# Optimization experiments

Measured on AMD Instinct MI355X. Metric: run time of the kernel, lower is better.

## Reference

```python
import jax, jax.numpy as jnp
import numpy as np

H, W = 5, 11          # fixed spatial map from ConvLSTM2D((5,11), ...)
P = H * W             # 55 pixels; 1x1 convs are per-pixel linear layers
HC = 64               # hidden channels
IC = 2                # input channels
FC_DIMS = [2 * HC * P, 3400, 1000, 500, 50]  # 7040 -> 3400 -> 1000 -> 500 -> 50


def setup_inputs() -> dict:
    key = jax.random.key(0)
    ks = jax.random.split(key, 24)
    B, T = 32, 256
    s = 0.05
    d = {}
    d["x1"] = jax.random.normal(ks[0], (B, T, IC, H, W), jnp.float32)
    d["x2"] = jax.random.normal(ks[1], (B, T, IC, H, W), jnp.float32)
    # ConvLSTM cell params: 1x1 convs fused into (in, 4*HC) matrices, gate order i,f,o,g
    d["wx1"] = jax.random.normal(ks[2], (IC, 4 * HC), jnp.float32) * s
    d["wh1"] = jax.random.normal(ks[3], (HC, 4 * HC), jnp.float32) * s
    d["bx1"] = jax.random.normal(ks[4], (4 * HC,), jnp.float32) * s
    d["bh1"] = jax.random.normal(ks[5], (4 * HC,), jnp.float32) * s
    d["wx2"] = jax.random.normal(ks[6], (IC, 4 * HC), jnp.float32) * s
    d["wh2"] = jax.random.normal(ks[7], (HC, 4 * HC), jnp.float32) * s
    d["bx2"] = jax.random.normal(ks[8], (4 * HC,), jnp.float32) * s
    d["bh2"] = jax.random.normal(ks[9], (4 * HC,), jnp.float32) * s
    # FC stack (stored as (in,out) so y = x @ W + b, equivalent to torch Linear)
    for i in range(4):
        fan_in, fan_out = FC_DIMS[i], FC_DIMS[i + 1]
        lim = 1.0 / np.sqrt(fan_in)
        d[f"fw{i+2}"] = jax.random.uniform(ks[10 + 2 * i], (fan_in, fan_out), jnp.float32, -lim, lim)
        d[f"fb{i+2}"] = jax.random.uniform(ks[11 + 2 * i], (fan_out,), jnp.float32, -lim, lim)
    return d


def _cell_step(h, c, gx, wh, bh):
    # gx: (B,P,4*HC) precomputed x contribution; h,c: (B,P,HC)
    g = gx + h @ wh + bh
    i, f, o, gg = jnp.split(g, 4, axis=-1)
    c = jax.nn.sigmoid(f) * c + jax.nn.sigmoid(i) * jnp.tanh(gg)
    h = jax.nn.sigmoid(o) * jnp.tanh(c)
    return h, c


def _sub_forward(x, wx1, wh1, bx1, bh1, wx2, wh2, bx2, bh2,
                 fw2, fb2, fw3, fb3, fw4, fb4, fw5, fb5):
    B, T = x.shape[0], x.shape[1]
    # (B,T,C,H,W) -> (B,T,P,C): pixels become a batch dim for the 1x1 convs
    xs = x.transpose(0, 1, 3, 4, 2).reshape(B, T, P, IC)
    # Precompute all input-to-gate projections once (big batched GEMM)
    gx1 = jnp.einsum('btpc,cd->btpd', xs, wx1) + bx1            # cell1: forward in time
    gx2 = jnp.einsum('btpc,cd->btpd', xs[:, ::-1], wx2) + bx2   # cell2: reversed in time
    h0 = jnp.zeros((B, P, HC), x.dtype)

    def step(carry, g):
        h1, c1, h2, c2 = carry
        g1, g2 = g
        h1, c1 = _cell_step(h1, c1, g1, wh1, bh1)
        h2, c2 = _cell_step(h2, c2, g2, wh2, bh2)
        return (h1, c1, h2, c2), None

    (h1, _, h2, _), _ = jax.lax.scan(
        step, (h0, h0, h0, h0),
        (gx1.transpose(1, 0, 2, 3), gx2.transpose(1, 0, 2, 3)))

    # torch.cat((h1,h2),1) on (B,HC,H,W) then flatten -> channel-major layout
    out = jnp.concatenate([h1.transpose(0, 2, 1), h2.transpose(0, 2, 1)], axis=1).reshape(B, -1)
    out = out @ fw2 + fb2
    out = out @ fw3 + fb3
    out = out @ fw4 + fb4
    out = out @ fw5 + fb5
    return out


def reference(x1, x2, wx1, wh1, bx1, bh1, wx2, wh2, bx2, bh2,
              fw2, fb2, fw3, fb3, fw4, fb4, fw5, fb5):
    args = (wx1, wh1, bx1, bh1, wx2, wh2, bx2, bh2,
            fw2, fb2, fw3, fb3, fw4, fb4, fw5, fb5)
    out1 = _sub_forward(x1, *args)
    out2 = _sub_forward(x2, *args)
    return (out1, out2)
```

## Files before the change

### kernel.cpp

```cpp
#include <hip/hip_runtime.h>


#define T_STEPS 256
#define PIX 55
#define MT 16
#define TILES 110
#define LOG2E 1.4426950408889634f
#define FC_SUB 128
#define FC_GRP 16

typedef float f32x4 __attribute__((ext_vector_type(4)));
typedef __bf16 bf16x8 __attribute__((ext_vector_type(8)));
typedef __bf16 bf16x4 __attribute__((ext_vector_type(4)));

__global__ __launch_bounds__(256) void lstm_kernel(
    const float* __restrict__ x1, const float* __restrict__ x2,
    const float* __restrict__ wx1, const float* __restrict__ wh1,
    const float* __restrict__ bx1, const float* __restrict__ bh1,
    const float* __restrict__ wx2, const float* __restrict__ wh2,
    const float* __restrict__ bx2, const float* __restrict__ bh2,
    float* __restrict__ feat)
{
    int bid  = blockIdx.x;
    int tile = bid % TILES;
    int cc   = bid / TILES;
    int sub  = cc >> 1, cell = cc & 1;
    const float* x  = sub  ? x2  : x1;
    const float* wx = cell ? wx2 : wx1;
    const float* wh = cell ? wh2 : wh1;
    const float* bx = cell ? bx2 : bx1;
    const float* bh = cell ? bh2 : bh1;

    int tid  = threadIdx.x;
    int w    = tid >> 6;
    int l    = tid & 63;
    int quad = l >> 4;
    int c16  = l & 15;

    __shared__ float xl[MT * 514];
    __shared__ __align__(16) __bf16 hb[2][2][MT][72];

    {
        int seq0 = tile * MT;
        for (int i = 0; i < 32; ++i) {
            int idx = tid + 256 * i;
            int m = idx >> 9;
            int tc = idx & 511;
            int t = tc >> 1, c = tc & 1;
            int seq = seq0 + m;
            int b = seq / PIX, p = seq % PIX;
            xl[m * 514 + tc] = x[((b * T_STEPS + t) * 2 + c) * PIX + p];
        }
    }
    {
        __bf16* hz = &hb[0][0][0][0];
        for (int i = tid; i < 2 * 2 * MT * 72; i += 256) hz[i] = (__bf16)0.0f;
    }

    bf16x8 Whi[4][2], Wlo[4][2];
    float btot[4][4], wxa[4][4], wxb[4][4];
#pragma unroll
    for (int g = 0; g < 4; ++g) {
        int col = 64 * g + 16 * w + c16;
#pragma unroll
        for (int r = 0; r < 4; ++r) {
            int u = 64 * g + 16 * w + 4 * quad + r;
            btot[g][r] = bx[u] + bh[u];
            wxa[g][r]  = wx[u];
            wxb[g][r]  = wx[256 + u];
        }
#pragma unroll
        for (int q = 0; q < 2; ++q) {
#pragma unroll
            for (int j = 0; j < 8; ++j) {
                int k = 32 * q + 8 * quad + j;
                float wv = wh[k * 256 + col];
                __bf16 hi = (__bf16)wv;
                Whi[g][q][j] = hi;
                Wlo[g][q][j] = (__bf16)(wv - (float)hi);
            }
        }
    }

    float cst[4]  = {0.f, 0.f, 0.f, 0.f};
    float hfin[4] = {0.f, 0.f, 0.f, 0.f};

    __syncthreads();

    for (int t = 0; t < T_STEPS; ++t) {
        int rb = t & 1, wb = rb ^ 1;
        int tx = cell ? (T_STEPS - 1 - t) : t;

        bf16x8 Bh[2], Bl[2];
#pragma unroll
        for (int q = 0; q < 2; ++q) {
            Bh[q] = *(const bf16x8*)&hb[rb][0][c16][32 * q + 8 * quad];
            Bl[q] = *(const bf16x8*)&hb[rb][1][c16][32 * q + 8 * quad];
        }
        float2 xv = *(const float2*)&xl[c16 * 514 + tx * 2];

        f32x4 acc[4];
#pragma unroll
        for (int g = 0; g < 4; ++g) {
#pragma unroll
            for (int r = 0; r < 4; ++r)
                acc[g][r] = fmaf(xv.y, wxb[g][r], fmaf(xv.x, wxa[g][r], btot[g][r]));
        }
#pragma unroll
        for (int g = 0; g < 4; ++g) {
            acc[g] = __builtin_amdgcn_mfma_f32_16x16x32_bf16(Whi[g][0], Bh[0], acc[g], 0, 0, 0);
            acc[g] = __builtin_amdgcn_mfma_f32_16x16x32_bf16(Whi[g][1], Bh[1], acc[g], 0, 0, 0);
            acc[g] = __builtin_amdgcn_mfma_f32_16x16x32_bf16(Wlo[g][0], Bh[0], acc[g], 0, 0, 0);
            acc[g] = __builtin_amdgcn_mfma_f32_16x16x32_bf16(Wlo[g][1], Bh[1], acc[g], 0, 0, 0);
            acc[g] = __builtin_amdgcn_mfma_f32_16x16x32_bf16(Whi[g][0], Bl[0], acc[g], 0, 0, 0);
            acc[g] = __builtin_amdgcn_mfma_f32_16x16x32_bf16(Whi[g][1], Bl[1], acc[g], 0, 0, 0);
        }

        bf16x4 ph, pl;
#pragma unroll
        for (int r = 0; r < 4; ++r) {
            float iv = acc[0][r], fv = acc[1][r], ov = acc[2][r], gv = acc[3][r];
            float ei = __builtin_amdgcn_exp2f(-LOG2E * iv);
            float ef = __builtin_amdgcn_exp2f(-LOG2E * fv);
            float eo = __builtin_amdgcn_exp2f(-LOG2E * ov);
            float eg = __builtin_amdgcn_exp2f(-2.0f * LOG2E * gv);
            float sf  = __builtin_amdgcn_rcpf(1.0f + ef);
            float itg = (1.0f - eg) * __builtin_amdgcn_rcpf((1.0f + ei) * (1.0f + eg));
            float c   = fmaf(sf, cst[r], itg);
            cst[r] = c;
            float ec = __builtin_amdgcn_exp2f(-2.0f * LOG2E * c);
            float h  = (1.0f - ec) * __builtin_amdgcn_rcpf((1.0f + eo) * (1.0f + ec));
            hfin[r] = h;
            __bf16 hi = (__bf16)h;
            ph[r] = hi;
            pl[r] = (__bf16)(h - (float)hi);
        }
        *(bf16x4*)&hb[wb][0][c16][16 * w + 4 * quad] = ph;
        *(bf16x4*)&hb[wb][1][c16][16 * w + 4 * quad] = pl;
        __syncthreads();
    }

    {
        int seq = tile * MT + c16;
        int b = seq / PIX, p = seq % PIX;
#pragma unroll
        for (int r = 0; r < 4; ++r) {
            int u = 16 * w + 4 * quad + r;
            feat[(size_t)(sub * 32 + b) * 7040 + (cell * 64 + u) * PIX + p] = hfin[r];
        }
    }
}

__global__ __launch_bounds__(256) void fc_gemm(const float* __restrict__ A,
                                               const float* __restrict__ W,
                                               float* __restrict__ part,
                                               int K, int N, int kchunk) {
    __shared__ __align__(16) float al[FC_SUB * 68];
    int tid = threadIdx.x;
    int l   = tid & 63;
    int wv  = tid >> 6;
    int k0   = blockIdx.y * kchunk;
    int kend = min(K, k0 + kchunk);

    int n  = blockIdx.x * 64 + l;
    int ne = min(n, N - 1);

    float acc[16];
#pragma unroll
    for (int i = 0; i < 16; ++i) acc[i] = 0.0f;

    for (int ks = k0; ks < kend; ks += FC_SUB) {
        int kcur = min(FC_SUB, kend - ks);
        __syncthreads();
        if (kcur == FC_SUB) {
#pragma unroll
            for (int i = 0; i < 32; ++i) {
                int idx = tid + 256 * i;
                int m = idx >> 7, kc = idx & 127;
                al[kc * 68 + m] = A[(size_t)m * K + ks + kc];
            }
        } else {
#pragma unroll
            for (int i = 0; i < 32; ++i) {
                int idx = tid + 256 * i;
                int m = idx >> 7, kc = idx & 127;
                if (kc < kcur) al[kc * 68 + m] = A[(size_t)m * K + ks + kc];
            }
        }
        __syncthreads();

        const float* wr = W + (size_t)ks * N + ne;
        int kc0 = 0;
        for (; kc0 + FC_GRP <= kcur; kc0 += FC_GRP) {
            float wbuf[FC_GRP];
#pragma unroll
            for (int j = 0; j < FC_GRP; ++j)
                wbuf[j] = wr[(size_t)(kc0 + j) * N];
#pragma unroll
            for (int j = 0; j < FC_GRP; ++j) {
                const float4* ap = (const float4*)&al[(kc0 + j) * 68 + 16 * wv];
#pragma unroll
                for (int i = 0; i < 4; ++i) {
                    float4 a = ap[i];
                    acc[4 * i + 0] = fmaf(a.x, wbuf[j], acc[4 * i + 0]);
                    acc[4 * i + 1] = fmaf(a.y, wbuf[j], acc[4 * i + 1]);
                    acc[4 * i + 2] = fmaf(a.z, wbuf[j], acc[4 * i + 2]);
                    acc[4 * i + 3] = fmaf(a.w, wbuf[j], acc[4 * i + 3]);
                }
            }
        }
        for (; kc0 < kcur; ++kc0) {
            float wvv = wr[(size_t)kc0 * N];
            const float4* ap = (const float4*)&al[kc0 * 68 + 16 * wv];
#pragma unroll
            for (int i = 0; i < 4; ++i) {
                float4 a = ap[i];
                acc[4 * i + 0] = fmaf(a.x, wvv, acc[4 * i + 0]);
                acc[4 * i + 1] = fmaf(a.y, wvv, acc[4 * i + 1]);
                acc[4 * i + 2] = fmaf(a.z, wvv, acc[4 * i + 2]);
                acc[4 * i + 3] = fmaf(a.w, wvv, acc[4 * i + 3]);
            }
        }
    }

    if (n < N) {
        float* pr = part + (size_t)blockIdx.y * 64 * N + n;
#pragma unroll
        for (int i = 0; i < 16; ++i)
            pr[(size_t)(16 * wv + i) * N] = acc[i];
    }
}

__global__ __launch_bounds__(256) void fc_reduce(const float* __restrict__ part,
                                                 const float* __restrict__ bias,
                                                 float* __restrict__ out,
                                                 int S, int N) {
    int n = blockIdx.x * 256 + threadIdx.x;
    int m = blockIdx.y;
    if (n >= N) return;
    float s = bias[n];
    for (int i = 0; i < S; ++i)
        s += part[(size_t)i * 64 * N + (size_t)m * N + n];
    out[(size_t)m * N + n] = s;
}

extern "C" void kernel_launch(void* const* d_in, const int* in_sizes, int n_in,
                              void* d_out, int out_size, void* d_ws, size_t ws_size,
                              hipStream_t stream) {
    const float* x1  = (const float*)d_in[0];
    const float* x2  = (const float*)d_in[1];
    const float* wx1 = (const float*)d_in[2];
    const float* wh1 = (const float*)d_in[3];
    const float* bx1 = (const float*)d_in[4];
    const float* bh1 = (const float*)d_in[5];
    const float* wx2 = (const float*)d_in[6];
    const float* wh2 = (const float*)d_in[7];
    const float* bx2 = (const float*)d_in[8];
    const float* bh2 = (const float*)d_in[9];
    const float* fw2 = (const float*)d_in[10];
    const float* fb2 = (const float*)d_in[11];
    const float* fw3 = (const float*)d_in[12];
    const float* fb3 = (const float*)d_in[13];
    const float* fw4 = (const float*)d_in[14];
    const float* fb4 = (const float*)d_in[15];
    const float* fw5 = (const float*)d_in[16];
    const float* fb5 = (const float*)d_in[17];

    char* ws = (char*)d_ws;
    float* feat = (float*)ws;
    float* t1   = feat + (size_t)64 * 7040;
    float* t2   = t1   + (size_t)64 * 3400;
    float* t3   = t2   + (size_t)64 * 1000;
    float* part = t3   + (size_t)64 * 500;
    float* o    = (float*)d_out;

    lstm_kernel<<<dim3(440), dim3(256), 0, stream>>>(
        x1, x2, wx1, wh1, bx1, bh1, wx2, wh2, bx2, bh2, feat);

    fc_gemm<<<dim3(54, 14), dim3(256), 0, stream>>>(feat, fw2, part, 7040, 3400, 512);
    fc_reduce<<<dim3(14, 64), dim3(256), 0, stream>>>(part, fb2, t1, 14, 3400);

    fc_gemm<<<dim3(16, 27), dim3(256), 0, stream>>>(t1, fw3, part, 3400, 1000, 128);
    fc_reduce<<<dim3(4, 64), dim3(256), 0, stream>>>(part, fb3, t2, 27, 1000);

    fc_gemm<<<dim3(8, 8), dim3(256), 0, stream>>>(t2, fw4, part, 1000, 500, 128);
    fc_reduce<<<dim3(2, 64), dim3(256), 0, stream>>>(part, fb4, t3, 8, 500);

    fc_gemm<<<dim3(1, 4), dim3(256), 0, stream>>>(t3, fw5, part, 500, 50, 128);
    fc_reduce<<<dim3(1, 64), dim3(256), 0, stream>>>(part, fb5, o, 4, 50);
}
```

Baseline: 590.6 us.

## Prefetch LSTM inputs, interleave MFMA chains, and widen FC GEMM to two columns

The LSTM step loop now loads the next timestep's input before the barrier and is unrolled by two. The MFMA calls are reordered so the four gate accumulators form independent chains instead of six dependent calls per gate, and the exponentials are computed in a separate batch before the gate math. The FC GEMM has each lane compute two output columns with float2 weight loads and stores, which halves the grid width and reuses each shared-memory A value twice. This raises register pressure and assumes N is even for aligned float2 access.

```diff
diff --git a/kernel.cpp b/kernel.cpp
--- a/kernel.cpp
+++ b/kernel.cpp
@@ -86,10 +86,11 @@
     float hfin[4] = {0.f, 0.f, 0.f, 0.f};
 
     __syncthreads();
-
+    float2 xv = *(const float2*)&xl[c16 * 514 + (cell ? (T_STEPS - 1) : 0) * 2];
+
+#pragma unroll 2
     for (int t = 0; t < T_STEPS; ++t) {
         int rb = t & 1, wb = rb ^ 1;
-        int tx = cell ? (T_STEPS - 1 - t) : t;
 
         bf16x8 Bh[2], Bl[2];
 #pragma unroll
@@ -97,7 +98,6 @@
             Bh[q] = *(const bf16x8*)&hb[rb][0][c16][32 * q + 8 * quad];
             Bl[q] = *(const bf16x8*)&hb[rb][1][c16][32 * q + 8 * quad];
         }
-        float2 xv = *(const float2*)&xl[c16 * 514 + tx * 2];
 
         f32x4 acc[4];
 #pragma unroll
@@ -107,29 +107,42 @@
                 acc[g][r] = fmaf(xv.y, wxb[g][r], fmaf(xv.x, wxa[g][r], btot[g][r]));
         }
 #pragma unroll
-        for (int g = 0; g < 4; ++g) {
+        for (int g = 0; g < 4; ++g)
             acc[g] = __builtin_amdgcn_mfma_f32_16x16x32_bf16(Whi[g][0], Bh[0], acc[g], 0, 0, 0);
+#pragma unroll
+        for (int g = 0; g < 4; ++g)
             acc[g] = __builtin_amdgcn_mfma_f32_16x16x32_bf16(Whi[g][1], Bh[1], acc[g], 0, 0, 0);
+#pragma unroll
+        for (int g = 0; g < 4; ++g)
             acc[g] = __builtin_amdgcn_mfma_f32_16x16x32_bf16(Wlo[g][0], Bh[0], acc[g], 0, 0, 0);
+#pragma unroll
+        for (int g = 0; g < 4; ++g)
             acc[g] = __builtin_amdgcn_mfma_f32_16x16x32_bf16(Wlo[g][1], Bh[1], acc[g], 0, 0, 0);
+#pragma unroll
+        for (int g = 0; g < 4; ++g)
             acc[g] = __builtin_amdgcn_mfma_f32_16x16x32_bf16(Whi[g][0], Bl[0], acc[g], 0, 0, 0);
+#pragma unroll
+        for (int g = 0; g < 4; ++g)
             acc[g] = __builtin_amdgcn_mfma_f32_16x16x32_bf16(Whi[g][1], Bl[1], acc[g], 0, 0, 0);
+
+        float ei[4], ef[4], eo[4], eg[4];
+#pragma unroll
+        for (int r = 0; r < 4; ++r) {
+            ei[r] = __builtin_amdgcn_exp2f(-LOG2E * acc[0][r]);
+            ef[r] = __builtin_amdgcn_exp2f(-LOG2E * acc[1][r]);
+            eo[r] = __builtin_amdgcn_exp2f(-LOG2E * acc[2][r]);
+            eg[r] = __builtin_amdgcn_exp2f(-2.0f * LOG2E * acc[3][r]);
         }
 
         bf16x4 ph, pl;
 #pragma unroll
         for (int r = 0; r < 4; ++r) {
-            float iv = acc[0][r], fv = acc[1][r], ov = acc[2][r], gv = acc[3][r];
-            float ei = __builtin_amdgcn_exp2f(-LOG2E * iv);
-            float ef = __builtin_amdgcn_exp2f(-LOG2E * fv);
-            float eo = __builtin_amdgcn_exp2f(-LOG2E * ov);
-            float eg = __builtin_amdgcn_exp2f(-2.0f * LOG2E * gv);
-            float sf  = __builtin_amdgcn_rcpf(1.0f + ef);
-            float itg = (1.0f - eg) * __builtin_amdgcn_rcpf((1.0f + ei) * (1.0f + eg));
+            float sf  = __builtin_amdgcn_rcpf(1.0f + ef[r]);
+            float itg = (1.0f - eg[r]) * __builtin_amdgcn_rcpf((1.0f + ei[r]) * (1.0f + eg[r]));
             float c   = fmaf(sf, cst[r], itg);
             cst[r] = c;
             float ec = __builtin_amdgcn_exp2f(-2.0f * LOG2E * c);
-            float h  = (1.0f - ec) * __builtin_amdgcn_rcpf((1.0f + eo) * (1.0f + ec));
+            float h  = (1.0f - ec) * __builtin_amdgcn_rcpf((1.0f + eo[r]) * (1.0f + ec));
             hfin[r] = h;
             __bf16 hi = (__bf16)h;
             ph[r] = hi;
@@ -137,6 +150,11 @@
         }
         *(bf16x4*)&hb[wb][0][c16][16 * w + 4 * quad] = ph;
         *(bf16x4*)&hb[wb][1][c16][16 * w + 4 * quad] = pl;
+
+        {
+            int txn = (cell ? (T_STEPS - 2 - t) : (t + 1)) & 255;
+            xv = *(const float2*)&xl[c16 * 514 + txn * 2];
+        }
         __syncthreads();
     }
 
@@ -162,12 +180,12 @@
     int k0   = blockIdx.y * kchunk;
     int kend = min(K, k0 + kchunk);
 
-    int n  = blockIdx.x * 64 + l;
-    int ne = min(n, N - 1);
-
-    float acc[16];
-#pragma unroll
-    for (int i = 0; i < 16; ++i) acc[i] = 0.0f;
+    int n  = blockIdx.x * 128 + 2 * l;
+    int ne = min(n, N - 2);
+
+    float2 acc[16];
+#pragma unroll
+    for (int i = 0; i < 16; ++i) acc[i] = make_float2(0.0f, 0.0f);
 
     for (int ks = k0; ks < kend; ks += FC_SUB) {
         int kcur = min(FC_SUB, kend - ks);
@@ -192,33 +210,41 @@
         const float* wr = W + (size_t)ks * N + ne;
         int kc0 = 0;
         for (; kc0 + FC_GRP <= kcur; kc0 += FC_GRP) {
-            float wbuf[FC_GRP];
+            float2 wbuf[FC_GRP];
 #pragma unroll
             for (int j = 0; j < FC_GRP; ++j)
-                wbuf[j] = wr[(size_t)(kc0 + j) * N];
+                wbuf[j] = *(const float2*)&wr[(size_t)(kc0 + j) * N];
 #pragma unroll
             for (int j = 0; j < FC_GRP; ++j) {
                 const float4* ap = (const float4*)&al[(kc0 + j) * 68 + 16 * wv];
 #pragma unroll
                 for (int i = 0; i < 4; ++i) {
                     float4 a = ap[i];
-                    acc[4 * i + 0] = fmaf(a.x, wbuf[j], acc[4 * i + 0]);
-                    acc[4 * i + 1] = fmaf(a.y, wbuf[j], acc[4 * i + 1]);
-                    acc[4 * i + 2] = fmaf(a.z, wbuf[j], acc[4 * i + 2]);
-                    acc[4 * i + 3] = fmaf(a.w, wbuf[j], acc[4 * i + 3]);
+                    acc[4 * i + 0].x = fmaf(a.x, wbuf[j].x, acc[4 * i + 0].x);
+                    acc[4 * i + 0].y = fmaf(a.x, wbuf[j].y, acc[4 * i + 0].y);
+                    acc[4 * i + 1].x = fmaf(a.y, wbuf[j].x, acc[4 * i + 1].x);
+                    acc[4 * i + 1].y = fmaf(a.y, wbuf[j].y, acc[4 * i + 1].y);
+                    acc[4 * i + 2].x = fmaf(a.z, wbuf[j].x, acc[4 * i + 2].x);
+                    acc[4 * i + 2].y = fmaf(a.z, wbuf[j].y, acc[4 * i + 2].y);
+                    acc[4 * i + 3].x = fmaf(a.w, wbuf[j].x, acc[4 * i + 3].x);
+                    acc[4 * i + 3].y = fmaf(a.w, wbuf[j].y, acc[4 * i + 3].y);
                 }
             }
         }
         for (; kc0 < kcur; ++kc0) {
-            float wvv = wr[(size_t)kc0 * N];
+            float2 wvv = *(const float2*)&wr[(size_t)kc0 * N];
             const float4* ap = (const float4*)&al[kc0 * 68 + 16 * wv];
 #pragma unroll
             for (int i = 0; i < 4; ++i) {
                 float4 a = ap[i];
-                acc[4 * i + 0] = fmaf(a.x, wvv, acc[4 * i + 0]);
-                acc[4 * i + 1] = fmaf(a.y, wvv, acc[4 * i + 1]);
-                acc[4 * i + 2] = fmaf(a.z, wvv, acc[4 * i + 2]);
-                acc[4 * i + 3] = fmaf(a.w, wvv, acc[4 * i + 3]);
+                acc[4 * i + 0].x = fmaf(a.x, wvv.x, acc[4 * i + 0].x);
+                acc[4 * i + 0].y = fmaf(a.x, wvv.y, acc[4 * i + 0].y);
+                acc[4 * i + 1].x = fmaf(a.y, wvv.x, acc[4 * i + 1].x);
+                acc[4 * i + 1].y = fmaf(a.y, wvv.y, acc[4 * i + 1].y);
+                acc[4 * i + 2].x = fmaf(a.z, wvv.x, acc[4 * i + 2].x);
+                acc[4 * i + 2].y = fmaf(a.z, wvv.y, acc[4 * i + 2].y);
+                acc[4 * i + 3].x = fmaf(a.w, wvv.x, acc[4 * i + 3].x);
+                acc[4 * i + 3].y = fmaf(a.w, wvv.y, acc[4 * i + 3].y);
             }
         }
     }
@@ -227,7 +253,7 @@
         float* pr = part + (size_t)blockIdx.y * 64 * N + n;
 #pragma unroll
         for (int i = 0; i < 16; ++i)
-            pr[(size_t)(16 * wv + i) * N] = acc[i];
+            *(float2*)&pr[(size_t)(16 * wv + i) * N] = acc[i];
     }
 }
 
@@ -277,13 +303,13 @@
     lstm_kernel<<<dim3(440), dim3(256), 0, stream>>>(
         x1, x2, wx1, wh1, bx1, bh1, wx2, wh2, bx2, bh2, feat);
 
-    fc_gemm<<<dim3(54, 14), dim3(256), 0, stream>>>(feat, fw2, part, 7040, 3400, 512);
+    fc_gemm<<<dim3(27, 14), dim3(256), 0, stream>>>(feat, fw2, part, 7040, 3400, 512);
     fc_reduce<<<dim3(14, 64), dim3(256), 0, stream>>>(part, fb2, t1, 14, 3400);
 
-    fc_gemm<<<dim3(16, 27), dim3(256), 0, stream>>>(t1, fw3, part, 3400, 1000, 128);
+    fc_gemm<<<dim3(8, 27), dim3(256), 0, stream>>>(t1, fw3, part, 3400, 1000, 128);
     fc_reduce<<<dim3(4, 64), dim3(256), 0, stream>>>(part, fb3, t2, 27, 1000);
 
-    fc_gemm<<<dim3(8, 8), dim3(256), 0, stream>>>(t2, fw4, part, 1000, 500, 128);
+    fc_gemm<<<dim3(4, 8), dim3(256), 0, stream>>>(t2, fw4, part, 1000, 500, 128);
     fc_reduce<<<dim3(2, 64), dim3(256), 0, stream>>>(part, fb4, t3, 8, 500);
 
     fc_gemm<<<dim3(1, 4), dim3(256), 0, stream>>>(t3, fw5, part, 500, 50, 128);
```

Result: slower. 772.5 us (+30.8%).
